# Kernel optimization log

Measured on AMD Instinct MI355X. Metric: run time of the kernel, lower is better.

Reference implementation:

```python
import jax, jax.numpy as jnp
import numpy as np
import math

PATCHES = [(2, 2), (4, 4), (8, 8), (16, 16)]  # (width, height) per scale
D_MODEL = 256
EPS = 1e-5


def setup_inputs() -> dict:
    key = jax.random.key(0)
    ks = jax.random.split(key, 12)
    b, c, h, w = 4, D_MODEL, 128, 128
    s = 1.0 / math.sqrt(c)
    inp = {
        'x': jax.random.normal(ks[0], (b, c, h, w), jnp.float32),
        'y': jax.random.normal(ks[1], (b, c, h, w), jnp.float32),
        'Wq': jax.random.normal(ks[2], (c, c), jnp.float32) * s,
        'bq': jnp.zeros((c,), jnp.float32),
        'Wk': jax.random.normal(ks[3], (c, c), jnp.float32) * s,
        'bk': jnp.zeros((c,), jnp.float32),
        'Wv': jax.random.normal(ks[4], (c, c), jnp.float32) * s,
        'bv': jnp.zeros((c,), jnp.float32),
        'Wo': jax.random.normal(ks[5], (c, c, 3, 3), jnp.float32) * (1.0 / math.sqrt(c * 9)),
        'bo': jnp.zeros((c,), jnp.float32),
        'gamma': jnp.ones((c,), jnp.float32),
        'beta': jnp.zeros((c,), jnp.float32),
    }
    return inp


def _conv1x1(x, W, b):
    # 1x1 conv == channel matmul
    return jnp.einsum('oc,bchw->bohw', W, x) + b[None, :, None, None]


def _windowed_attention(q, k, v, ww, hh):
    # q,k,v: [b, d_k, h, w] -> windows of (hh, ww), tokens = out_h*out_w
    b, d_k, h, w = q.shape
    out_h, out_w = h // hh, w // ww

    def to_tokens(t):
        t = t.reshape(b, d_k, out_h, hh, out_w, ww)
        t = t.transpose(0, 2, 4, 1, 3, 5)  # b, out_h, out_w, d_k, hh, ww
        return t.reshape(b, out_h * out_w, d_k * hh * ww)

    qt, kt, vt = to_tokens(q), to_tokens(k), to_tokens(v)
    scale = 1.0 / math.sqrt(qt.shape[-1])
    scores = jnp.einsum('bnd,bmd->bnm', qt, kt) * scale
    p = jax.nn.softmax(scores, axis=-1)
    out = jnp.einsum('bnm,bmd->bnd', p, vt)
    out = out.reshape(b, out_h, out_w, d_k, hh, ww)
    out = out.transpose(0, 3, 1, 4, 2, 5).reshape(b, d_k, h, w)
    return out


def reference(x, y, Wq, bq, Wk, bk, Wv, bv, Wo, bo, gamma, beta):
    b, c, h, w = x.shape
    n_scales = len(PATCHES)
    d_k = c // n_scales

    q_all = _conv1x1(x, Wq, bq)
    k_all = _conv1x1(y, Wk, bk)
    v_all = _conv1x1(y, Wv, bv)

    outs = []
    for i, (ww, hh) in enumerate(PATCHES):
        sl = slice(i * d_k, (i + 1) * d_k)
        outs.append(_windowed_attention(q_all[:, sl], k_all[:, sl], v_all[:, sl], ww, hh))
    out = jnp.concatenate(outs, axis=1)  # [b, c, h, w]

    # output_linear: Conv3x3 (pad 1) -> BatchNorm2d (batch stats) -> LeakyReLU(0.2)
    z = jax.lax.conv_general_dilated(
        out, Wo, window_strides=(1, 1), padding='SAME',
        dimension_numbers=('NCHW', 'OIHW', 'NCHW')) + bo[None, :, None, None]
    mean = jnp.mean(z, axis=(0, 2, 3), keepdims=True)
    var = jnp.var(z, axis=(0, 2, 3), keepdims=True)
    zn = (z - mean) * jax.lax.rsqrt(var + EPS)
    zn = zn * gamma[None, :, None, None] + beta[None, :, None, None]
    return jnp.where(zn >= 0, zn, 0.2 * zn)
```

## Files before the change

### kernel.cpp

```cpp
#include <hip/hip_runtime.h>
#include <math.h>

#define BN 4
#define CC 256
#define HH_ 128
#define WW_ 128
#define HWP (HH_*WW_)
#define TOK (64*HWP)


typedef __attribute__((ext_vector_type(8))) short bf16x8;
typedef __attribute__((ext_vector_type(4))) float f32x4;

__device__ __forceinline__ float bf2f(unsigned short u) {
    return __uint_as_float(((unsigned)u) << 16);
}
__device__ __forceinline__ unsigned short f2bf(float f) {
    unsigned u = __float_as_uint(f);
    u += 0x7FFF + ((u >> 16) & 1);
    return (unsigned short)(u >> 16);
}
__device__ __forceinline__ void load4f(const unsigned short* p, float o[4]) {
    ushort4 v = *(const ushort4*)p;
    o[0] = bf2f(v.x); o[1] = bf2f(v.y); o[2] = bf2f(v.z); o[3] = bf2f(v.w);
}
__device__ __forceinline__ float ld1(const unsigned short* p) { return bf2f(*p); }
__device__ __forceinline__ float ld1(const float* p) { return *p; }
__device__ __forceinline__ void st1(unsigned short* p, float v) { *p = f2bf(v); }
__device__ __forceinline__ void st1(float* p, float v) { *p = v; }

#define LDS_STRIDE 72

struct Tile32 { uint4 v[4]; };

__device__ __forceinline__ Tile32 load_tile_bf16(
    const unsigned short* src, size_t stride, int t)
{
    int r = t >> 1, kc = (t & 1) * 32;
    const uint4* sp = (const uint4*)(src + (size_t)r * stride + kc);
    Tile32 o;
    o.v[0] = sp[0]; o.v[1] = sp[1]; o.v[2] = sp[2]; o.v[3] = sp[3];
    return o;
}

__device__ __forceinline__ Tile32 load_tile_f32(
    const float* src, size_t stride, int t)
{
    int r = t >> 1, kc = (t & 1) * 32;
    const float4* sp = (const float4*)(src + (size_t)r * stride + kc);
    unsigned short tmp[32];
    #pragma unroll
    for (int i = 0; i < 8; i++) {
        float4 v = sp[i];
        tmp[i*4+0] = f2bf(v.x); tmp[i*4+1] = f2bf(v.y);
        tmp[i*4+2] = f2bf(v.z); tmp[i*4+3] = f2bf(v.w);
    }
    Tile32 o;
    const uint4* tp = (const uint4*)tmp;
    o.v[0] = tp[0]; o.v[1] = tp[1]; o.v[2] = tp[2]; o.v[3] = tp[3];
    return o;
}

__device__ __forceinline__ void store_tile(
    unsigned short* lds, const Tile32& d, int t)
{
    int r = t >> 1, kc = (t & 1) * 32;
    uint4* dp = (uint4*)&lds[r * LDS_STRIDE + kc];
    dp[0] = d.v[0]; dp[1] = d.v[1]; dp[2] = d.v[2]; dp[3] = d.v[3];
}

__device__ __forceinline__ void mfma_iter(
    const unsigned short* As, const unsigned short* Bs,
    int wm, int wn, int lr, int quad, f32x4 acc[4][4])
{
    #pragma unroll
    for (int s = 0; s < 2; s++) {
        bf16x8 af[4], bfr[4];
        #pragma unroll
        for (int i = 0; i < 4; i++)
            af[i] = *(const bf16x8*)&As[(wm*64 + i*16 + lr) * LDS_STRIDE + s*32 + quad*8];
        #pragma unroll
        for (int j = 0; j < 4; j++)
            bfr[j] = *(const bf16x8*)&Bs[(wn*64 + j*16 + lr) * LDS_STRIDE + s*32 + quad*8];
        #pragma unroll
        for (int i = 0; i < 4; i++)
            #pragma unroll
            for (int j = 0; j < 4; j++)
                acc[i][j] = __builtin_amdgcn_mfma_f32_16x16x32_bf16(
                    af[i], bfr[j], acc[i][j], 0, 0, 0);
    }
}

__global__ __launch_bounds__(256) void zero_kernel(float* __restrict__ p)
{
    p[blockIdx.x * 256 + threadIdx.x] = 0.f;
}

__global__ __launch_bounds__(256) void nchw_to_nhwc(
    const float* __restrict__ x, const float* __restrict__ y,
    unsigned short* __restrict__ xt, unsigned short* __restrict__ yt)
{
    __shared__ unsigned short T[64 * 72];
    int z = blockIdx.z;
    int b = z & 3, which = z >> 2;
    const float* src = (which ? y : x) + (size_t)b * CC * HWP;
    unsigned short* dst = (which ? yt : xt) + (size_t)b * HWP * CC;
    int p0 = blockIdx.x * 64, c0 = blockIdx.y * 64;
    int t = threadIdx.x;

    int cl = t >> 2, pc = (t & 3) * 16;
    #pragma unroll
    for (int e = 0; e < 16; e += 4) {
        float4 v = *(const float4*)&src[(size_t)(c0 + cl) * HWP + p0 + pc + e];
        T[(pc + e + 0) * 72 + cl] = f2bf(v.x);
        T[(pc + e + 1) * 72 + cl] = f2bf(v.y);
        T[(pc + e + 2) * 72 + cl] = f2bf(v.z);
        T[(pc + e + 3) * 72 + cl] = f2bf(v.w);
    }
    __syncthreads();
    int p = t >> 2, cc = (t & 3) * 16;
    uint4 a = *(uint4*)&T[p * 72 + cc];
    uint4 bsec = *(uint4*)&T[p * 72 + cc + 8];
    uint4* dp = (uint4*)&dst[(size_t)(p0 + p) * CC + c0 + cc];
    dp[0] = a; dp[1] = bsec;
}

__global__ __launch_bounds__(256) void wpack_kernel(
    const float* __restrict__ Wo, unsigned short* __restrict__ wpack)
{
    int o = blockIdx.x, c = threadIdx.x;
    const float* wr = Wo + ((size_t)o * CC + c) * 9;
    #pragma unroll
    for (int tap = 0; tap < 9; tap++)
        wpack[((size_t)o * 9 + tap) * CC + c] = f2bf(wr[tap]);
}

__global__ __launch_bounds__(256) void proj_gemm(
    const unsigned short* __restrict__ xt, const unsigned short* __restrict__ yt,
    const float* __restrict__ Wq, const float* __restrict__ bq,
    const float* __restrict__ Wk, const float* __restrict__ bk,
    const float* __restrict__ Wv, const float* __restrict__ bv,
    unsigned short* __restrict__ qt, unsigned short* __restrict__ kt,
    unsigned short* __restrict__ vt)
{
    __shared__ unsigned short As[128 * LDS_STRIDE], Bs[128 * LDS_STRIDE];
    int z = blockIdx.z, b = z & 3, which = z >> 2;
    const unsigned short* src = (which == 0) ? xt : yt;
    const float* Wm   = (which == 0) ? Wq : (which == 1 ? Wk : Wv);
    const float* bias = (which == 0) ? bq : (which == 1 ? bk : bv);
    unsigned short* outp = (which == 0) ? qt : (which == 1 ? kt : vt);

    int m0 = blockIdx.y * 128;
    int n0 = blockIdx.x * 128;
    const float* A = Wm + (size_t)m0 * CC;
    const unsigned short* B = src + ((size_t)b * HWP + n0) * CC;

    int t = threadIdx.x, w = t >> 6, lane = t & 63;
    int quad = lane >> 4, lr = lane & 15, wm = w >> 1, wn = w & 1;

    f32x4 acc[4][4];
    #pragma unroll
    for (int i = 0; i < 4; i++)
        #pragma unroll
        for (int j = 0; j < 4; j++) acc[i][j] = (f32x4){0.f, 0.f, 0.f, 0.f};

    for (int k0 = 0; k0 < CC; k0 += 64) {
        Tile32 ta = load_tile_f32(A + k0, CC, t);
        Tile32 tb = load_tile_bf16(B + k0, CC, t);
        __syncthreads();
        store_tile(As, ta, t); store_tile(Bs, tb, t);
        __syncthreads();
        mfma_iter(As, Bs, wm, wn, lr, quad, acc);
    }

    #pragma unroll
    for (int i = 0; i < 4; i++) {
        int obase = m0 + wm * 64 + i * 16 + quad * 4;
        #pragma unroll
        for (int rr = 0; rr < 4; rr++) {
            int o = obase + rr;
            int s = o >> 6, lg = s + 1;
            int ch = o & 63;
            float bia = bias[o];
            unsigned short* ob = outp + ((size_t)s * 4 + b) * TOK;
            #pragma unroll
            for (int j = 0; j < 4; j++) {
                int p = n0 + wn * 64 + j * 16 + lr;
                int yy = p >> 7, xx = p & 127;
                int oy = yy >> lg, wy = yy & ((1 << lg) - 1);
                int ox = xx >> lg, wx = xx & ((1 << lg) - 1);
                int tokn = (oy << (7 - lg)) + ox;
                int didx = (ch << (2 * lg)) + (wy << lg) + wx;
                size_t idx;
                if (which == 2 && s < 3)
                    idx = ((size_t)didx << (14 - 2 * lg)) + tokn;
                else
                    idx = ((size_t)tokn << (6 + 2 * lg)) + didx;
                ob[idx] = f2bf(acc[i][j][rr] + bia);
            }
        }
    }
}

#define PS_STRIDE 136

__global__ __launch_bounds__(512) void flash0(
    const unsigned short* __restrict__ qt, const unsigned short* __restrict__ kt,
    const unsigned short* __restrict__ vt, unsigned short* __restrict__ aot)
{
    __shared__ unsigned short Ps[64 * PS_STRIDE];
    __shared__ unsigned short Bs[256 * LDS_STRIDE];

    int L = blockIdx.x;
    int xcd = L & 7, slot = L >> 3;
    int b = xcd >> 1;
    int q0 = (slot + 32 * (xcd & 1)) * 64;

    const unsigned short* Qb = qt + (size_t)b * TOK;
    const unsigned short* Kb = kt + (size_t)b * TOK;
    const unsigned short* Vb = vt + (size_t)b * TOK;

    int t = threadIdx.x, w = t >> 6, lane = t & 63;
    int quad = lane >> 4, lr = lane & 15;
    int wm = w >> 2, wn = w & 3;

    bf16x8 aq[4][2][2];
    #pragma unroll
    for (int k = 0; k < 4; k++)
        #pragma unroll
        for (int s = 0; s < 2; s++)
            #pragma unroll
            for (int i = 0; i < 2; i++)
                aq[k][s][i] = *(const bf16x8*)&Qb[
                    (size_t)(q0 + wm*32 + i*16 + lr) * 256 + k*64 + s*32 + quad*8];

    f32x4 acc_o[2][4];
    #pragma unroll
    for (int i = 0; i < 2; i++)
        #pragma unroll
        for (int j = 0; j < 4; j++) acc_o[i][j] = (f32x4){0.f, 0.f, 0.f, 0.f};
    float rsum[2][4] = {};

    const float SC = 1.f / 16.f;
    int sr = t >> 1, sc_ = (t & 1) * 32;

    for (int kv0 = 0; kv0 < 4096; kv0 += 128) {
        f32x4 acc_s[2][2];
        #pragma unroll
        for (int i = 0; i < 2; i++)
            #pragma unroll
            for (int j = 0; j < 2; j++) acc_s[i][j] = (f32x4){0.f, 0.f, 0.f, 0.f};

        #pragma unroll
        for (int kp = 0; kp < 2; kp++) {
            __syncthreads();
            {
                const uint4* sp = (const uint4*)&Kb[
                    (size_t)(kv0 + (sr & 127)) * 256 + kp*128 + (sr >> 7)*64 + sc_];
                uint4* dp = (uint4*)&Bs[sr * LDS_STRIDE + sc_];
                dp[0] = sp[0]; dp[1] = sp[1]; dp[2] = sp[2]; dp[3] = sp[3];
            }
            __syncthreads();
            #pragma unroll
            for (int t2 = 0; t2 < 2; t2++)
                #pragma unroll
                for (int s = 0; s < 2; s++) {
                    bf16x8 bfr[2];
                    #pragma unroll
                    for (int j = 0; j < 2; j++)
                        bfr[j] = *(const bf16x8*)&Bs[
                            (t2*128 + wn*32 + j*16 + lr) * LDS_STRIDE + s*32 + quad*8];
                    #pragma unroll
                    for (int i = 0; i < 2; i++)
                        #pragma unroll
                        for (int j = 0; j < 2; j++)
                            acc_s[i][j] = __builtin_amdgcn_mfma_f32_16x16x32_bf16(
                                aq[kp*2 + t2][s][i], bfr[j], acc_s[i][j], 0, 0, 0);
                }
        }

        #pragma unroll
        for (int i = 0; i < 2; i++)
            #pragma unroll
            for (int j = 0; j < 2; j++)
                #pragma unroll
                for (int rr = 0; rr < 4; rr++) {
                    float e = __expf(acc_s[i][j][rr] * SC);
                    Ps[(wm*32 + i*16 + quad*4 + rr) * PS_STRIDE + wn*32 + j*16 + lr]
                        = f2bf(e);
                    rsum[i][rr] += e;
                }

        #pragma unroll
        for (int ks = 0; ks < 2; ks++) {
            __syncthreads();
            {
                const uint4* sp = (const uint4*)&Vb[
                    (size_t)sr * 4096 + kv0 + ks*64 + sc_];
                uint4* dp = (uint4*)&Bs[sr * LDS_STRIDE + sc_];
                dp[0] = sp[0]; dp[1] = sp[1]; dp[2] = sp[2]; dp[3] = sp[3];
            }
            __syncthreads();
            #pragma unroll
            for (int s = 0; s < 2; s++) {
                bf16x8 pa[2], vb[4];
                #pragma unroll
                for (int i = 0; i < 2; i++)
                    pa[i] = *(const bf16x8*)&Ps[
                        (wm*32 + i*16 + lr) * PS_STRIDE + ks*64 + s*32 + quad*8];
                #pragma unroll
                for (int j = 0; j < 4; j++)
                    vb[j] = *(const bf16x8*)&Bs[
                        (wn*64 + j*16 + lr) * LDS_STRIDE + s*32 + quad*8];
                #pragma unroll
                for (int i = 0; i < 2; i++)
                    #pragma unroll
                    for (int j = 0; j < 4; j++)
                        acc_o[i][j] = __builtin_amdgcn_mfma_f32_16x16x32_bf16(
                            pa[i], vb[j], acc_o[i][j], 0, 0, 0);
            }
        }
    }

    __syncthreads();
    float* rsred = (float*)Ps;
    #pragma unroll
    for (int i = 0; i < 2; i++)
        #pragma unroll
        for (int rr = 0; rr < 4; rr++) {
            float v = rsum[i][rr];
            v += __shfl_xor(v, 1); v += __shfl_xor(v, 2);
            v += __shfl_xor(v, 4); v += __shfl_xor(v, 8);
            if (lr == 0)
                rsred[wn*64 + wm*32 + i*16 + quad*4 + rr] = v;
        }
    __syncthreads();
    #pragma unroll
    for (int i = 0; i < 2; i++)
        #pragma unroll
        for (int rr = 0; rr < 4; rr++) {
            int tl = wm*32 + i*16 + quad*4 + rr;
            float inv = 1.f / (rsred[tl] + rsred[64 + tl]
                             + rsred[128 + tl] + rsred[192 + tl]);
            int tokn = q0 + tl;
            int oy = tokn >> 6, ox = tokn & 63;
            #pragma unroll
            for (int j = 0; j < 4; j++) {
                int d = wn*64 + j*16 + lr;
                int ch = d >> 2, wp = d & 3;
                int yy = oy*2 + (wp >> 1), xx = ox*2 + (wp & 1);
                aot[((size_t)b * HWP + yy * WW_ + xx) * CC + ch]
                    = f2bf(acc_o[i][j][rr] * inv);
            }
        }
}

template<int NTOK, int DD>
__global__ __launch_bounds__(256) void s_gemm_exp(
    const unsigned short* __restrict__ Qb, const unsigned short* __restrict__ Kb,
    unsigned short* __restrict__ S0, float* __restrict__ rsg, float sc)
{
    __shared__ unsigned short As[128 * LDS_STRIDE], Bs[128 * LDS_STRIDE];
    int bz = blockIdx.z;
    int m0 = blockIdx.y * 128, n0 = blockIdx.x * 128;
    const unsigned short* Q = Qb + (size_t)bz * TOK + (size_t)m0 * DD;
    const unsigned short* K = Kb + (size_t)bz * TOK + (size_t)n0 * DD;
    unsigned short* S = S0 + (size_t)bz * NTOK * NTOK;
    float* rs = rsg + (size_t)bz * NTOK;

    int t = threadIdx.x, w = t >> 6, lane = t & 63;
    int quad = lane >> 4, lr = lane & 15, wm = w >> 1, wn = w & 1;

    f32x4 acc[4][4];
    #pragma unroll
    for (int i = 0; i < 4; i++)
        #pragma unroll
        for (int j = 0; j < 4; j++) acc[i][j] = (f32x4){0.f, 0.f, 0.f, 0.f};

    for (int k0 = 0; k0 < DD; k0 += 64) {
        Tile32 ta = load_tile_bf16(Q + k0, DD, t);
        Tile32 tb = load_tile_bf16(K + k0, DD, t);
        __syncthreads();
        store_tile(As, ta, t); store_tile(Bs, tb, t);
        __syncthreads();
        mfma_iter(As, Bs, wm, wn, lr, quad, acc);
    }

    #pragma unroll
    for (int i = 0; i < 4; i++) {
        int m = m0 + wm * 64 + i * 16 + quad * 4;
        float rsum[4] = {0.f, 0.f, 0.f, 0.f};
        #pragma unroll
        for (int j = 0; j < 4; j++) {
            int n = n0 + wn * 64 + j * 16 + lr;
            #pragma unroll
            for (int rr = 0; rr < 4; rr++) {
                float e = __expf(acc[i][j][rr] * sc);
                S[(size_t)(m + rr) * NTOK + n] = f2bf(e);
                rsum[rr] += e;
            }
        }
        #pragma unroll
        for (int rr = 0; rr < 4; rr++) {
            float v = rsum[rr];
            v += __shfl_xor(v, 1);
            v += __shfl_xor(v, 2);
            v += __shfl_xor(v, 4);
            v += __shfl_xor(v, 8);
            if (lr == 0) atomicAdd(&rs[m + rr], v);
        }
    }
}

template<int NTOK, int DD, int LG, int CH0>
__global__ __launch_bounds__(256) void o_gemm(
    const unsigned short* __restrict__ Pb, const unsigned short* __restrict__ Vb,
    const float* __restrict__ rsg, unsigned short* __restrict__ aot, int b0)
{
    __shared__ unsigned short As[128 * LDS_STRIDE], Bs[128 * LDS_STRIDE];
    int bz = blockIdx.z, b = b0 + bz;
    int m0 = blockIdx.y * 128, n0 = blockIdx.x * 128;
    const unsigned short* P = Pb + (size_t)bz * NTOK * NTOK + (size_t)m0 * NTOK;
    const unsigned short* V = Vb + (size_t)bz * TOK + (size_t)n0 * NTOK;
    const float* rs = rsg + (size_t)bz * NTOK;

    int t = threadIdx.x, w = t >> 6, lane = t & 63;
    int quad = lane >> 4, lr = lane & 15, wm = w >> 1, wn = w & 1;

    f32x4 acc[4][4];
    #pragma unroll
    for (int i = 0; i < 4; i++)
        #pragma unroll
        for (int j = 0; j < 4; j++) acc[i][j] = (f32x4){0.f, 0.f, 0.f, 0.f};

    for (int k0 = 0; k0 < NTOK; k0 += 64) {
        Tile32 ta = load_tile_bf16(P + k0, NTOK, t);
        Tile32 tb = load_tile_bf16(V + k0, NTOK, t);
        __syncthreads();
        store_tile(As, ta, t); store_tile(Bs, tb, t);
        __syncthreads();
        mfma_iter(As, Bs, wm, wn, lr, quad, acc);
    }

    #pragma unroll
    for (int i = 0; i < 4; i++) {
        int tb0 = m0 + wm * 64 + i * 16 + quad * 4;
        #pragma unroll
        for (int rr = 0; rr < 4; rr++) {
            int tokn = tb0 + rr;
            float inv = 1.f / rs[tokn];
            int oy = tokn >> (7 - LG), ox = tokn & ((1 << (7 - LG)) - 1);
            #pragma unroll
            for (int j = 0; j < 4; j++) {
                int d = n0 + wn * 64 + j * 16 + lr;
                int ch = d >> (2 * LG);
                int r2 = d & ((1 << (2 * LG)) - 1);
                int wy = r2 >> LG, wx = r2 & ((1 << LG) - 1);
                int yy = (oy << LG) + wy, xx = (ox << LG) + wx;
                aot[((size_t)b * HWP + yy * WW_ + xx) * CC + CH0 + ch] =
                    f2bf(acc[i][j][rr] * inv);
            }
        }
    }
}

__global__ __launch_bounds__(256) void s2_partial(
    const unsigned short* __restrict__ Qb, const unsigned short* __restrict__ Kb,
    float* __restrict__ S2p)
{
    __shared__ unsigned short As[128 * LDS_STRIDE], Bs[128 * LDS_STRIDE];
    int z = blockIdx.z, b = z >> 3, sp = z & 7;
    int m0 = blockIdx.y * 128, n0 = blockIdx.x * 128;
    const unsigned short* Q = Qb + (size_t)b * TOK + (size_t)m0 * 4096;
    const unsigned short* K = Kb + (size_t)b * TOK + (size_t)n0 * 4096;
    float* So = S2p + ((size_t)(sp * 4 + b)) * 65536;

    int t = threadIdx.x, w = t >> 6, lane = t & 63;
    int quad = lane >> 4, lr = lane & 15, wm = w >> 1, wn = w & 1;

    f32x4 acc[4][4];
    #pragma unroll
    for (int i = 0; i < 4; i++)
        #pragma unroll
        for (int j = 0; j < 4; j++) acc[i][j] = (f32x4){0.f, 0.f, 0.f, 0.f};

    int kend = sp * 512 + 512;
    for (int k0 = sp * 512; k0 < kend; k0 += 64) {
        Tile32 ta = load_tile_bf16(Q + k0, 4096, t);
        Tile32 tb = load_tile_bf16(K + k0, 4096, t);
        __syncthreads();
        store_tile(As, ta, t); store_tile(Bs, tb, t);
        __syncthreads();
        mfma_iter(As, Bs, wm, wn, lr, quad, acc);
    }

    #pragma unroll
    for (int i = 0; i < 4; i++) {
        int m = m0 + wm * 64 + i * 16 + quad * 4;
        #pragma unroll
        for (int j = 0; j < 4; j++) {
            int n = n0 + wn * 64 + j * 16 + lr;
            #pragma unroll
            for (int rr = 0; rr < 4; rr++)
                So[(size_t)(m + rr) * 256 + n] = acc[i][j][rr];
        }
    }
}

__global__ __launch_bounds__(256) void s2_finish(
    const float* __restrict__ S2p, unsigned short* __restrict__ Sbf,
    float* __restrict__ rs2, float sc)
{
    int row = blockIdx.x, b = blockIdx.y, t = threadIdx.x;
    float v = 0.f;
    #pragma unroll
    for (int sp = 0; sp < 8; sp++)
        v += S2p[((size_t)(sp * 4 + b)) * 65536 + row * 256 + t];
    float e = __expf(v * sc);
    Sbf[((size_t)b * 65536) + row * 256 + t] = f2bf(e);
    __shared__ float red[256];
    red[t] = e; __syncthreads();
    for (int s = 128; s > 0; s >>= 1) {
        if (t < s) red[t] += red[t + s];
        __syncthreads();
    }
    if (t == 0) rs2[b * 256 + row] = red[0];
}

__device__ __forceinline__ Tile32 load_tile_conv(
    const unsigned short* aob, int ys, int dx, int cbase, int t)
{
    int r = t >> 1, kc = (t & 1) * 32;
    int xs = r + dx;
    Tile32 o;
    if (ys >= 0 && ys < HH_ && xs >= 0 && xs < WW_) {
        const uint4* sp = (const uint4*)(aob + ((size_t)ys * WW_ + xs) * CC + cbase + kc);
        o.v[0] = sp[0]; o.v[1] = sp[1]; o.v[2] = sp[2]; o.v[3] = sp[3];
    } else {
        uint4 zz = make_uint4(0, 0, 0, 0);
        o.v[0] = zz; o.v[1] = zz; o.v[2] = zz; o.v[3] = zz;
    }
    return o;
}

__global__ __launch_bounds__(256) void conv_gemm(
    const unsigned short* __restrict__ aot, const unsigned short* __restrict__ wpack,
    const float* __restrict__ bo, float* __restrict__ zout,
    float* __restrict__ stats)
{
    __shared__ unsigned short As[128 * LDS_STRIDE], Bs[128 * LDS_STRIDE];
    int yrow = blockIdx.x;
    int o0 = blockIdx.y * 128;
    int b = blockIdx.z;
    const unsigned short* aob = aot + (size_t)b * HWP * CC;
    const unsigned short* wsrc = wpack + (size_t)o0 * 2304;

    int t = threadIdx.x, w = t >> 6, lane = t & 63;
    int quad = lane >> 4, lr = lane & 15, wm = w >> 1, wn = w & 1;

    f32x4 acc[4][4];
    #pragma unroll
    for (int i = 0; i < 4; i++)
        #pragma unroll
        for (int j = 0; j < 4; j++) acc[i][j] = (f32x4){0.f, 0.f, 0.f, 0.f};

    for (int tap = 0; tap < 9; tap++) {
        int dy = tap / 3 - 1, dx = tap % 3 - 1;
        int ys = yrow + dy;
        for (int cb = 0; cb < CC; cb += 64) {
            Tile32 ta = load_tile_bf16(wsrc + tap * CC + cb, 2304, t);
            Tile32 tb = load_tile_conv(aob, ys, dx, cb, t);
            __syncthreads();
            store_tile(As, ta, t); store_tile(Bs, tb, t);
            __syncthreads();
            mfma_iter(As, Bs, wm, wn, lr, quad, acc);
        }
    }

    #pragma unroll
    for (int i = 0; i < 4; i++) {
        #pragma unroll
        for (int rr = 0; rr < 4; rr++) {
            int o = o0 + wm * 64 + i * 16 + quad * 4 + rr;
            float bia = bo[o];
            float s1 = 0.f, s2v = 0.f;
            #pragma unroll
            for (int j = 0; j < 4; j++) {
                int x = wn * 64 + j * 16 + lr;
                float v = acc[i][j][rr] + bia;
                zout[((size_t)(b * CC + o)) * HWP + yrow * WW_ + x] = v;
                s1 += v; s2v = fmaf(v, v, s2v);
            }
            s1 += __shfl_xor(s1, 1); s2v += __shfl_xor(s2v, 1);
            s1 += __shfl_xor(s1, 2); s2v += __shfl_xor(s2v, 2);
            s1 += __shfl_xor(s1, 4); s2v += __shfl_xor(s2v, 4);
            s1 += __shfl_xor(s1, 8); s2v += __shfl_xor(s2v, 8);
            if (lr == 0) {
                atomicAdd(&stats[o], s1);
                atomicAdd(&stats[CC + o], s2v);
            }
        }
    }
}

__global__ __launch_bounds__(256) void stats_finalize(
    float* __restrict__ stats, const float* __restrict__ gamma,
    const float* __restrict__ beta)
{
    int c = threadIdx.x;
    const float inv_n = 1.f / (BN * HWP);
    float mean = stats[c] * inv_n;
    float var = stats[CC + c] * inv_n - mean * mean;
    float rstd = rsqrtf(var + 1e-5f);
    float gs = gamma[c] * rstd;
    stats[c] = gs;
    stats[CC + c] = beta[c] - mean * gs;
}

__global__ __launch_bounds__(256) void s3_kernel(
    const unsigned short* __restrict__ Qb, const unsigned short* __restrict__ Kb,
    float* __restrict__ S, float sc)
{
    const int N = 64, D = 16384, KLEN = 1024;
    int b = blockIdx.z >> 4, kc = blockIdx.z & 15;
    const unsigned short* Q = Qb + (size_t)b * TOK;
    const unsigned short* K = Kb + (size_t)b * TOK;
    float* Sb = S + (size_t)b * N * N;
    int k0 = kc * KLEN;

    __shared__ float As[16][64], Bs[16][64];
    int t = threadIdx.x, tx = t & 15, ty = t >> 4, r = t >> 2, q = t & 3;

    float acc[4][4] = {};
    for (int kk = k0; kk < k0 + KLEN; kk += 16) {
        float a4[4], b4[4];
        load4f(&Q[(size_t)r * D + kk + q * 4], a4);
        load4f(&K[(size_t)r * D + kk + q * 4], b4);
        __syncthreads();
        As[q*4+0][r] = a4[0]; As[q*4+1][r] = a4[1]; As[q*4+2][r] = a4[2]; As[q*4+3][r] = a4[3];
        Bs[q*4+0][r] = b4[0]; Bs[q*4+1][r] = b4[1]; Bs[q*4+2][r] = b4[2]; Bs[q*4+3][r] = b4[3];
        __syncthreads();
        #pragma unroll
        for (int k = 0; k < 16; k++) {
            float4 af = *(const float4*)&As[k][ty*4];
            float4 bf = *(const float4*)&Bs[k][tx*4];
            float ar[4] = {af.x, af.y, af.z, af.w};
            float br[4] = {bf.x, bf.y, bf.z, bf.w};
            #pragma unroll
            for (int ii = 0; ii < 4; ii++)
                #pragma unroll
                for (int jj = 0; jj < 4; jj++)
                    acc[ii][jj] = fmaf(ar[ii], br[jj], acc[ii][jj]);
        }
    }

    #pragma unroll
    for (int ii = 0; ii < 4; ii++)
        #pragma unroll
        for (int jj = 0; jj < 4; jj++)
            atomicAdd(&Sb[(size_t)(ty * 4 + ii) * N + tx * 4 + jj], acc[ii][jj] * sc);
}

template<typename T>
__global__ __launch_bounds__(256) void softmax_kernel(T* __restrict__ S, int n)
{
    int b = blockIdx.y;
    int row = blockIdx.x;
    T* rp = S + (size_t)b * n * n + (size_t)row * n;
    __shared__ float red[256];
    int t = threadIdx.x;

    float m = -1e30f;
    for (int j = t; j < n; j += 256) m = fmaxf(m, ld1(&rp[j]));
    red[t] = m; __syncthreads();
    for (int s = 128; s > 0; s >>= 1) { if (t < s) red[t] = fmaxf(red[t], red[t + s]); __syncthreads(); }
    m = red[0]; __syncthreads();

    float sum = 0.f;
    for (int j = t; j < n; j += 256) { float e = __expf(ld1(&rp[j]) - m); st1(&rp[j], e); sum += e; }
    red[t] = sum; __syncthreads();
    for (int s = 128; s > 0; s >>= 1) { if (t < s) red[t] += red[t + s]; __syncthreads(); }
    float inv = 1.f / red[0];
    for (int j = t; j < n; j += 256) st1(&rp[j], ld1(&rp[j]) * inv);
}

__global__ __launch_bounds__(256) void o3_kernel(
    const float* __restrict__ P, const unsigned short* __restrict__ Vb,
    unsigned short* __restrict__ aot)
{
    const int N = 64, D = 16384, LG = 4, CH0 = 192;
    int bz = blockIdx.z;
    const float* Pb = P + (size_t)bz * N * N;
    const unsigned short* V = Vb + (size_t)bz * TOK;
    int i0 = blockIdx.x * 64, d0 = blockIdx.y * 64;

    __shared__ float Ps[16][64];
    __shared__ float Vs[16][64];
    int t = threadIdx.x, tx = t & 15, ty = t >> 4, r = t >> 2, q = t & 3;
    int vr = t >> 4, vq = t & 15;

    float acc[4][4] = {};
    for (int j0 = 0; j0 < N; j0 += 16) {
        float p4[4], v4[4];
        float4 pv = *(const float4*)&Pb[(size_t)(i0 + r) * N + j0 + q * 4];
        p4[0] = pv.x; p4[1] = pv.y; p4[2] = pv.z; p4[3] = pv.w;
        load4f(&V[(size_t)(j0 + vr) * D + d0 + vq * 4], v4);
        __syncthreads();
        Ps[q*4+0][r] = p4[0]; Ps[q*4+1][r] = p4[1]; Ps[q*4+2][r] = p4[2]; Ps[q*4+3][r] = p4[3];
        Vs[vr][vq*4+0] = v4[0]; Vs[vr][vq*4+1] = v4[1]; Vs[vr][vq*4+2] = v4[2]; Vs[vr][vq*4+3] = v4[3];
        __syncthreads();
        #pragma unroll
        for (int k = 0; k < 16; k++) {
            float4 pf = *(const float4*)&Ps[k][ty*4];
            float4 vf = *(const float4*)&Vs[k][tx*4];
            float pr[4] = {pf.x, pf.y, pf.z, pf.w};
            float vrr[4] = {vf.x, vf.y, vf.z, vf.w};
            #pragma unroll
            for (int ii = 0; ii < 4; ii++)
                #pragma unroll
                for (int jj = 0; jj < 4; jj++)
                    acc[ii][jj] = fmaf(pr[ii], vrr[jj], acc[ii][jj]);
        }
    }

    #pragma unroll
    for (int ii = 0; ii < 4; ii++) {
        int tokn = i0 + ty * 4 + ii;
        int oy = tokn >> (7 - LG), ox = tokn & ((1 << (7 - LG)) - 1);
        #pragma unroll
        for (int jj = 0; jj < 4; jj++) {
            int d = d0 + tx * 4 + jj;
            int ch = d >> (2 * LG);
            int r2 = d & ((1 << (2 * LG)) - 1);
            int wy = r2 >> LG, wx = r2 & ((1 << LG) - 1);
            int yy = (oy << LG) + wy, xx = (ox << LG) + wx;
            aot[((size_t)bz * HWP + yy * WW_ + xx) * CC + CH0 + ch] = f2bf(acc[ii][jj]);
        }
    }
}

__global__ __launch_bounds__(256) void bn_apply_kernel(
    float* __restrict__ z, const float* __restrict__ stats)
{
    size_t i4 = (size_t)blockIdx.x * 256 + threadIdx.x;
    size_t idx = i4 * 4;
    int c = (int)((idx >> 14) & 255);
    float gs = stats[c], gb = stats[CC + c];
    float4 v = *(float4*)&z[idx];
    v.x = fmaf(v.x, gs, gb); v.y = fmaf(v.y, gs, gb);
    v.z = fmaf(v.z, gs, gb); v.w = fmaf(v.w, gs, gb);
    v.x = v.x >= 0.f ? v.x : 0.2f * v.x;
    v.y = v.y >= 0.f ? v.y : 0.2f * v.y;
    v.z = v.z >= 0.f ? v.z : 0.2f * v.z;
    v.w = v.w >= 0.f ? v.w : 0.2f * v.w;
    *(float4*)&z[idx] = v;
}

extern "C" void kernel_launch(void* const* d_in, const int* in_sizes, int n_in,
                              void* d_out, int out_size, void* d_ws, size_t ws_size,
                              hipStream_t stream)
{
    const float* x     = (const float*)d_in[0];
    const float* y     = (const float*)d_in[1];
    const float* Wq    = (const float*)d_in[2];
    const float* bq    = (const float*)d_in[3];
    const float* Wk    = (const float*)d_in[4];
    const float* bk    = (const float*)d_in[5];
    const float* Wv    = (const float*)d_in[6];
    const float* bv    = (const float*)d_in[7];
    const float* Wo    = (const float*)d_in[8];
    const float* bo    = (const float*)d_in[9];
    const float* gamma = (const float*)d_in[10];
    const float* beta  = (const float*)d_in[11];
    float* out = (float*)d_out;

    unsigned short* qt    = (unsigned short*)d_ws;
    unsigned short* kt    = qt + (size_t)16777216;
    unsigned short* vt    = kt + (size_t)16777216;
    unsigned short* aot   = vt + (size_t)16777216;
    unsigned short* Sbf   = aot + (size_t)16777216;
    unsigned short* wpack = Sbf + (size_t)16777216;
    float* stats = (float*)(wpack + (size_t)589824);
    float* S3    = stats + 512;
    float* rs0   = S3 + 16384;
    float* rs1   = rs0 + 16384;
    float* rs2   = rs1 + 4096;
    (void)rs0;
    unsigned short* xt = Sbf;
    unsigned short* yt = aot;
    float* S2p = (float*)d_out;

    dim3 blk(256);

    zero_kernel<<<dim3(150), blk, 0, stream>>>(stats);
    nchw_to_nhwc<<<dim3(256, 4, 8), blk, 0, stream>>>(x, y, xt, yt);
    wpack_kernel<<<dim3(256), blk, 0, stream>>>(Wo, wpack);

    proj_gemm<<<dim3(128, 2, 12), blk, 0, stream>>>(
        xt, yt, Wq, bq, Wk, bk, Wv, bv, qt, kt, vt);

    flash0<<<dim3(256), dim3(512), 0, stream>>>(qt, kt, vt, aot);

    s_gemm_exp<1024, 1024><<<dim3(8, 8, 4), blk, 0, stream>>>(
        qt + (size_t)4 * TOK, kt + (size_t)4 * TOK, Sbf, rs1, 1.f / 32.f);
    o_gemm<1024, 1024, 2, 64><<<dim3(8, 8, 4), blk, 0, stream>>>(
        Sbf, vt + (size_t)4 * TOK, rs1, aot, 0);

    s2_partial<<<dim3(2, 2, 32), blk, 0, stream>>>(
        qt + (size_t)8 * TOK, kt + (size_t)8 * TOK, S2p);
    s2_finish<<<dim3(256, 4), blk, 0, stream>>>(S2p, Sbf, rs2, 1.f / 64.f);
    o_gemm<256, 4096, 3, 128><<<dim3(32, 2, 4), blk, 0, stream>>>(
        Sbf, vt + (size_t)8 * TOK, rs2, aot, 0);

    s3_kernel<<<dim3(1, 1, 64), blk, 0, stream>>>(
        qt + (size_t)12 * TOK, kt + (size_t)12 * TOK, S3, 1.f / 128.f);
    softmax_kernel<float><<<dim3(64, 4), blk, 0, stream>>>(S3, 64);
    o3_kernel<<<dim3(1, 256, 4), blk, 0, stream>>>(S3, vt + (size_t)12 * TOK, aot);

    conv_gemm<<<dim3(128, 2, 4), blk, 0, stream>>>(aot, wpack, bo, out, stats);
    stats_finalize<<<dim3(1), blk, 0, stream>>>(stats, gamma, beta);
    bn_apply_kernel<<<dim3(16384), blk, 0, stream>>>(out, stats);
}
```

Before: 880.2 us.

## Use async LDS loads with swizzle, double-buffer GEMMs, split flash0 over KV

The GEMM kernels now load tiles with global_load_lds straight into XOR-swizzled, double-buffered LDS, so the next tile's fetch overlaps the current MFMA work. The QKV weights are pre-converted to bf16 by a new pack kernel so the projection can use the same path. flash0 is split into two KV halves across twice as many blocks, writing fp32 partials and atomically summed row sums, with a new combine kernel that normalises and scatters the output. This aims to cut load latency, bank conflicts and occupancy limits, but adds fp32 partial traffic, atomics and an extra launch.

```diff
diff --git a/kernel.cpp b/kernel.cpp
--- a/kernel.cpp
+++ b/kernel.cpp
@@ -29,6 +29,53 @@
 __device__ __forceinline__ void st1(unsigned short* p, float v) { *p = f2bf(v); }
 __device__ __forceinline__ void st1(float* p, float v) { *p = v; }
 
+__device__ __forceinline__ void gload16(const void* g, void* l) {
+    __builtin_amdgcn_global_load_lds(
+        (__attribute__((address_space(1))) void*)(g),
+        (__attribute__((address_space(3))) void*)(l), 16, 0, 0);
+}
+
+__device__ __forceinline__ void stage64(
+    const unsigned short* src, size_t strideElems, unsigned short* lds, int t)
+{
+    #pragma unroll
+    for (int k = 0; k < 4; k++) {
+        int n = t + k * 256;
+        int row = n >> 3, slot = n & 7;
+        const char* gp = (const char*)(src + (size_t)row * strideElems)
+                       + ((slot ^ (row & 7)) << 4);
+        gload16(gp, (char*)lds + n * 16);
+    }
+}
+
+__device__ __forceinline__ void mfma_iter_swz(
+    const unsigned short* As, const unsigned short* Bs,
+    int wm, int wn, int lr, int quad, f32x4 acc[4][4])
+{
+    #pragma unroll
+    for (int s = 0; s < 2; s++) {
+        bf16x8 af[4], bfr[4];
+        #pragma unroll
+        for (int i = 0; i < 4; i++) {
+            int row = wm*64 + i*16 + lr;
+            int off = (row << 7) + (s << 6) + (quad << 4);
+            af[i] = *(const bf16x8*)((const char*)As + (off ^ ((row & 7) << 4)));
+        }
+        #pragma unroll
+        for (int j = 0; j < 4; j++) {
+            int row = wn*64 + j*16 + lr;
+            int off = (row << 7) + (s << 6) + (quad << 4);
+            bfr[j] = *(const bf16x8*)((const char*)Bs + (off ^ ((row & 7) << 4)));
+        }
+        #pragma unroll
+        for (int i = 0; i < 4; i++)
+            #pragma unroll
+            for (int j = 0; j < 4; j++)
+                acc[i][j] = __builtin_amdgcn_mfma_f32_16x16x32_bf16(
+                    af[i], bfr[j], acc[i][j], 0, 0, 0);
+    }
+}
+
 #define LDS_STRIDE 72
 
 struct Tile32 { uint4 v[4]; };
@@ -40,24 +87,6 @@
     const uint4* sp = (const uint4*)(src + (size_t)r * stride + kc);
     Tile32 o;
     o.v[0] = sp[0]; o.v[1] = sp[1]; o.v[2] = sp[2]; o.v[3] = sp[3];
-    return o;
-}
-
-__device__ __forceinline__ Tile32 load_tile_f32(
-    const float* src, size_t stride, int t)
-{
-    int r = t >> 1, kc = (t & 1) * 32;
-    const float4* sp = (const float4*)(src + (size_t)r * stride + kc);
-    unsigned short tmp[32];
-    #pragma unroll
-    for (int i = 0; i < 8; i++) {
-        float4 v = sp[i];
-        tmp[i*4+0] = f2bf(v.x); tmp[i*4+1] = f2bf(v.y);
-        tmp[i*4+2] = f2bf(v.z); tmp[i*4+3] = f2bf(v.w);
-    }
-    Tile32 o;
-    const uint4* tp = (const uint4*)tmp;
-    o.v[0] = tp[0]; o.v[1] = tp[1]; o.v[2] = tp[2]; o.v[3] = tp[3];
     return o;
 }
 
@@ -135,24 +164,34 @@
         wpack[((size_t)o * 9 + tap) * CC + c] = f2bf(wr[tap]);
 }
 
+__global__ __launch_bounds__(256) void wqkv_pack(
+    const float* __restrict__ Wq, const float* __restrict__ Wk,
+    const float* __restrict__ Wv, unsigned short* __restrict__ Wb)
+{
+    int which = blockIdx.x;
+    const float* W = which == 0 ? Wq : (which == 1 ? Wk : Wv);
+    unsigned short* o = Wb + (size_t)which * 65536;
+    for (int i = threadIdx.x; i < 65536; i += 256)
+        o[i] = f2bf(W[i]);
+}
+
 __global__ __launch_bounds__(256) void proj_gemm(
     const unsigned short* __restrict__ xt, const unsigned short* __restrict__ yt,
-    const float* __restrict__ Wq, const float* __restrict__ bq,
-    const float* __restrict__ Wk, const float* __restrict__ bk,
-    const float* __restrict__ Wv, const float* __restrict__ bv,
+    const unsigned short* __restrict__ Wqkv,
+    const float* __restrict__ bq, const float* __restrict__ bk,
+    const float* __restrict__ bv,
     unsigned short* __restrict__ qt, unsigned short* __restrict__ kt,
     unsigned short* __restrict__ vt)
 {
-    __shared__ unsigned short As[128 * LDS_STRIDE], Bs[128 * LDS_STRIDE];
+    __shared__ unsigned short Asb[2][8192], Bsb[2][8192];
     int z = blockIdx.z, b = z & 3, which = z >> 2;
     const unsigned short* src = (which == 0) ? xt : yt;
-    const float* Wm   = (which == 0) ? Wq : (which == 1 ? Wk : Wv);
     const float* bias = (which == 0) ? bq : (which == 1 ? bk : bv);
     unsigned short* outp = (which == 0) ? qt : (which == 1 ? kt : vt);
 
     int m0 = blockIdx.y * 128;
     int n0 = blockIdx.x * 128;
-    const float* A = Wm + (size_t)m0 * CC;
+    const unsigned short* A = Wqkv + (size_t)which * 65536 + (size_t)m0 * CC;
     const unsigned short* B = src + ((size_t)b * HWP + n0) * CC;
 
     int t = threadIdx.x, w = t >> 6, lane = t & 63;
@@ -164,13 +203,18 @@
         #pragma unroll
         for (int j = 0; j < 4; j++) acc[i][j] = (f32x4){0.f, 0.f, 0.f, 0.f};
 
+    stage64(A, CC, Asb[0], t);
+    stage64(B, CC, Bsb[0], t);
+    __syncthreads();
+    int cur = 0;
     for (int k0 = 0; k0 < CC; k0 += 64) {
-        Tile32 ta = load_tile_f32(A + k0, CC, t);
-        Tile32 tb = load_tile_bf16(B + k0, CC, t);
+        if (k0 + 64 < CC) {
+            stage64(A + k0 + 64, CC, Asb[cur ^ 1], t);
+            stage64(B + k0 + 64, CC, Bsb[cur ^ 1], t);
+        }
+        mfma_iter_swz(Asb[cur], Bsb[cur], wm, wn, lr, quad, acc);
         __syncthreads();
-        store_tile(As, ta, t); store_tile(Bs, tb, t);
-        __syncthreads();
-        mfma_iter(As, Bs, wm, wn, lr, quad, acc);
+        cur ^= 1;
     }
 
     #pragma unroll
@@ -206,15 +250,19 @@
 
 __global__ __launch_bounds__(512) void flash0(
     const unsigned short* __restrict__ qt, const unsigned short* __restrict__ kt,
-    const unsigned short* __restrict__ vt, unsigned short* __restrict__ aot)
+    const unsigned short* __restrict__ vt, float* __restrict__ part,
+    float* __restrict__ rs0g)
 {
     __shared__ unsigned short Ps[64 * PS_STRIDE];
-    __shared__ unsigned short Bs[256 * LDS_STRIDE];
+    __shared__ unsigned short Bs[256 * 64];
 
     int L = blockIdx.x;
     int xcd = L & 7, slot = L >> 3;
     int b = xcd >> 1;
-    int q0 = (slot + 32 * (xcd & 1)) * 64;
+    int idx = slot + 64 * (xcd & 1);
+    int h = idx >> 6;
+    int q0 = (idx & 63) * 64;
+    int kvbase = h * 2048;
 
     const unsigned short* Qb = qt + (size_t)b * TOK;
     const unsigned short* Kb = kt + (size_t)b * TOK;
@@ -242,9 +290,8 @@
     float rsum[2][4] = {};
 
     const float SC = 1.f / 16.f;
-    int sr = t >> 1, sc_ = (t & 1) * 32;
-
-    for (int kv0 = 0; kv0 < 4096; kv0 += 128) {
+
+    for (int kv0 = kvbase; kv0 < kvbase + 2048; kv0 += 128) {
         f32x4 acc_s[2][2];
         #pragma unroll
         for (int i = 0; i < 2; i++)
@@ -254,22 +301,29 @@
         #pragma unroll
         for (int kp = 0; kp < 2; kp++) {
             __syncthreads();
-            {
-                const uint4* sp = (const uint4*)&Kb[
-                    (size_t)(kv0 + (sr & 127)) * 256 + kp*128 + (sr >> 7)*64 + sc_];
-                uint4* dp = (uint4*)&Bs[sr * LDS_STRIDE + sc_];
-                dp[0] = sp[0]; dp[1] = sp[1]; dp[2] = sp[2]; dp[3] = sp[3];
+            #pragma unroll
+            for (int k = 0; k < 4; k++) {
+                int n = t + k * 512;
+                int R = n >> 3, sl = n & 7;
+                int kl = R & 127, dsub = R >> 7;
+                const char* gp = (const char*)(Kb + (size_t)(kv0 + kl) * 256
+                                 + kp*128 + dsub*64) + ((sl ^ (R & 7)) << 4);
+                gload16(gp, (char*)Bs + n * 16);
             }
             __syncthreads();
+            __builtin_amdgcn_s_setprio(1);
             #pragma unroll
             for (int t2 = 0; t2 < 2; t2++)
                 #pragma unroll
                 for (int s = 0; s < 2; s++) {
                     bf16x8 bfr[2];
                     #pragma unroll
-                    for (int j = 0; j < 2; j++)
-                        bfr[j] = *(const bf16x8*)&Bs[
-                            (t2*128 + wn*32 + j*16 + lr) * LDS_STRIDE + s*32 + quad*8];
+                    for (int j = 0; j < 2; j++) {
+                        int row = t2*128 + wn*32 + j*16 + lr;
+                        int off = (row << 7) + (s << 6) + (quad << 4);
+                        bfr[j] = *(const bf16x8*)((const char*)Bs
+                                   + (off ^ ((row & 7) << 4)));
+                    }
                     #pragma unroll
                     for (int i = 0; i < 2; i++)
                         #pragma unroll
@@ -277,6 +331,7 @@
                             acc_s[i][j] = __builtin_amdgcn_mfma_f32_16x16x32_bf16(
                                 aq[kp*2 + t2][s][i], bfr[j], acc_s[i][j], 0, 0, 0);
                 }
+            __builtin_amdgcn_s_setprio(0);
         }
 
         #pragma unroll
@@ -294,13 +349,16 @@
         #pragma unroll
         for (int ks = 0; ks < 2; ks++) {
             __syncthreads();
-            {
-                const uint4* sp = (const uint4*)&Vb[
-                    (size_t)sr * 4096 + kv0 + ks*64 + sc_];
-                uint4* dp = (uint4*)&Bs[sr * LDS_STRIDE + sc_];
-                dp[0] = sp[0]; dp[1] = sp[1]; dp[2] = sp[2]; dp[3] = sp[3];
+            #pragma unroll
+            for (int k = 0; k < 4; k++) {
+                int n = t + k * 512;
+                int R = n >> 3, sl = n & 7;
+                const char* gp = (const char*)(Vb + (size_t)R * 4096 + kv0 + ks*64)
+                               + ((sl ^ (R & 7)) << 4);
+                gload16(gp, (char*)Bs + n * 16);
             }
             __syncthreads();
+            __builtin_amdgcn_s_setprio(1);
             #pragma unroll
             for (int s = 0; s < 2; s++) {
                 bf16x8 pa[2], vb[4];
@@ -309,9 +367,12 @@
                     pa[i] = *(const bf16x8*)&Ps[
                         (wm*32 + i*16 + lr) * PS_STRIDE + ks*64 + s*32 + quad*8];
                 #pragma unroll
-                for (int j = 0; j < 4; j++)
-                    vb[j] = *(const bf16x8*)&Bs[
-                        (wn*64 + j*16 + lr) * LDS_STRIDE + s*32 + quad*8];
+                for (int j = 0; j < 4; j++) {
+                    int row = wn*64 + j*16 + lr;
+                    int off = (row << 7) + (s << 6) + (quad << 4);
+                    vb[j] = *(const bf16x8*)((const char*)Bs
+                              + (off ^ ((row & 7) << 4)));
+                }
                 #pragma unroll
                 for (int i = 0; i < 2; i++)
                     #pragma unroll
@@ -319,11 +380,10 @@
                         acc_o[i][j] = __builtin_amdgcn_mfma_f32_16x16x32_bf16(
                             pa[i], vb[j], acc_o[i][j], 0, 0, 0);
             }
-        }
-    }
-
-    __syncthreads();
-    float* rsred = (float*)Ps;
+            __builtin_amdgcn_s_setprio(0);
+        }
+    }
+
     #pragma unroll
     for (int i = 0; i < 2; i++)
         #pragma unroll
@@ -332,27 +392,41 @@
             v += __shfl_xor(v, 1); v += __shfl_xor(v, 2);
             v += __shfl_xor(v, 4); v += __shfl_xor(v, 8);
             if (lr == 0)
-                rsred[wn*64 + wm*32 + i*16 + quad*4 + rr] = v;
-        }
-    __syncthreads();
+                atomicAdd(&rs0g[b * 4096 + q0 + wm*32 + i*16 + quad*4 + rr], v);
+        }
+    float* op = part + ((size_t)(h * 4 + b)) * TOK;
     #pragma unroll
     for (int i = 0; i < 2; i++)
         #pragma unroll
         for (int rr = 0; rr < 4; rr++) {
-            int tl = wm*32 + i*16 + quad*4 + rr;
-            float inv = 1.f / (rsred[tl] + rsred[64 + tl]
-                             + rsred[128 + tl] + rsred[192 + tl]);
-            int tokn = q0 + tl;
-            int oy = tokn >> 6, ox = tokn & 63;
-            #pragma unroll
-            for (int j = 0; j < 4; j++) {
-                int d = wn*64 + j*16 + lr;
-                int ch = d >> 2, wp = d & 3;
-                int yy = oy*2 + (wp >> 1), xx = ox*2 + (wp & 1);
-                aot[((size_t)b * HWP + yy * WW_ + xx) * CC + ch]
-                    = f2bf(acc_o[i][j][rr] * inv);
-            }
-        }
+            int tokl = wm*32 + i*16 + quad*4 + rr;
+            float* orow = op + (size_t)(q0 + tokl) * 256;
+            #pragma unroll
+            for (int j = 0; j < 4; j++)
+                orow[wn*64 + j*16 + lr] = acc_o[i][j][rr];
+        }
+}
+
+__global__ __launch_bounds__(256) void combine0f(
+    const float* __restrict__ part, const float* __restrict__ rs,
+    unsigned short* __restrict__ aot)
+{
+    int b = blockIdx.y;
+    int tok0 = blockIdx.x * 16;
+    const float* p0 = part + (size_t)b * TOK;
+    const float* p1 = part + (size_t)(4 + b) * TOK;
+    int t = threadIdx.x;
+    int w = t >> 6, ch = t & 63;
+    int wy = w >> 1, wx = w & 1;
+    #pragma unroll 4
+    for (int u = 0; u < 16; u++) {
+        int tok = tok0 + u;
+        size_t base = (size_t)tok * 256 + ch * 4 + w;
+        float v = (p0[base] + p1[base]) * (1.f / rs[b * 4096 + tok]);
+        int oy = tok >> 6, ox = tok & 63;
+        int yy = oy * 2 + wy, xx = ox * 2 + wx;
+        aot[((size_t)b * HWP + yy * WW_ + xx) * CC + ch] = f2bf(v);
+    }
 }
 
 template<int NTOK, int DD>
@@ -360,7 +434,7 @@
     const unsigned short* __restrict__ Qb, const unsigned short* __restrict__ Kb,
     unsigned short* __restrict__ S0, float* __restrict__ rsg, float sc)
 {
-    __shared__ unsigned short As[128 * LDS_STRIDE], Bs[128 * LDS_STRIDE];
+    __shared__ unsigned short Asb[2][8192], Bsb[2][8192];
     int bz = blockIdx.z;
     int m0 = blockIdx.y * 128, n0 = blockIdx.x * 128;
     const unsigned short* Q = Qb + (size_t)bz * TOK + (size_t)m0 * DD;
@@ -377,13 +451,18 @@
         #pragma unroll
         for (int j = 0; j < 4; j++) acc[i][j] = (f32x4){0.f, 0.f, 0.f, 0.f};
 
+    stage64(Q, DD, Asb[0], t);
+    stage64(K, DD, Bsb[0], t);
+    __syncthreads();
+    int cur = 0;
     for (int k0 = 0; k0 < DD; k0 += 64) {
-        Tile32 ta = load_tile_bf16(Q + k0, DD, t);
-        Tile32 tb = load_tile_bf16(K + k0, DD, t);
+        if (k0 + 64 < DD) {
+            stage64(Q + k0 + 64, DD, Asb[cur ^ 1], t);
+            stage64(K + k0 + 64, DD, Bsb[cur ^ 1], t);
+        }
+        mfma_iter_swz(Asb[cur], Bsb[cur], wm, wn, lr, quad, acc);
         __syncthreads();
-        store_tile(As, ta, t); store_tile(Bs, tb, t);
-        __syncthreads();
-        mfma_iter(As, Bs, wm, wn, lr, quad, acc);
+        cur ^= 1;
     }
 
     #pragma unroll
@@ -417,7 +496,7 @@
     const unsigned short* __restrict__ Pb, const unsigned short* __restrict__ Vb,
     const float* __restrict__ rsg, unsigned short* __restrict__ aot, int b0)
 {
-    __shared__ unsigned short As[128 * LDS_STRIDE], Bs[128 * LDS_STRIDE];
+    __shared__ unsigned short Asb[2][8192], Bsb[2][8192];
     int bz = blockIdx.z, b = b0 + bz;
     int m0 = blockIdx.y * 128, n0 = blockIdx.x * 128;
     const unsigned short* P = Pb + (size_t)bz * NTOK * NTOK + (size_t)m0 * NTOK;
@@ -433,13 +512,18 @@
         #pragma unroll
         for (int j = 0; j < 4; j++) acc[i][j] = (f32x4){0.f, 0.f, 0.f, 0.f};
 
+    stage64(P, NTOK, Asb[0], t);
+    stage64(V, NTOK, Bsb[0], t);
+    __syncthreads();
+    int cur = 0;
     for (int k0 = 0; k0 < NTOK; k0 += 64) {
-        Tile32 ta = load_tile_bf16(P + k0, NTOK, t);
-        Tile32 tb = load_tile_bf16(V + k0, NTOK, t);
+        if (k0 + 64 < NTOK) {
+            stage64(P + k0 + 64, NTOK, Asb[cur ^ 1], t);
+            stage64(V + k0 + 64, NTOK, Bsb[cur ^ 1], t);
+        }
+        mfma_iter_swz(Asb[cur], Bsb[cur], wm, wn, lr, quad, acc);
         __syncthreads();
-        store_tile(As, ta, t); store_tile(Bs, tb, t);
-        __syncthreads();
-        mfma_iter(As, Bs, wm, wn, lr, quad, acc);
+        cur ^= 1;
     }
 
     #pragma unroll
@@ -468,11 +552,11 @@
     const unsigned short* __restrict__ Qb, const unsigned short* __restrict__ Kb,
     float* __restrict__ S2p)
 {
-    __shared__ unsigned short As[128 * LDS_STRIDE], Bs[128 * LDS_STRIDE];
+    __shared__ unsigned short Asb[2][8192], Bsb[2][8192];
     int z = blockIdx.z, b = z >> 3, sp = z & 7;
     int m0 = blockIdx.y * 128, n0 = blockIdx.x * 128;
-    const unsigned short* Q = Qb + (size_t)b * TOK + (size_t)m0 * 4096;
-    const unsigned short* K = Kb + (size_t)b * TOK + (size_t)n0 * 4096;
+    const unsigned short* Q = Qb + (size_t)b * TOK + (size_t)m0 * 4096 + sp * 512;
+    const unsigned short* K = Kb + (size_t)b * TOK + (size_t)n0 * 4096 + sp * 512;
     float* So = S2p + ((size_t)(sp * 4 + b)) * 65536;
 
     int t = threadIdx.x, w = t >> 6, lane = t & 63;
@@ -484,14 +568,18 @@
         #pragma unroll
         for (int j = 0; j < 4; j++) acc[i][j] = (f32x4){0.f, 0.f, 0.f, 0.f};
 
-    int kend = sp * 512 + 512;
-    for (int k0 = sp * 512; k0 < kend; k0 += 64) {
-        Tile32 ta = load_tile_bf16(Q + k0, 4096, t);
-        Tile32 tb = load_tile_bf16(K + k0, 4096, t);
+    stage64(Q, 4096, Asb[0], t);
+    stage64(K, 4096, Bsb[0], t);
+    __syncthreads();
+    int cur = 0;
+    for (int k0 = 0; k0 < 512; k0 += 64) {
+        if (k0 + 64 < 512) {
+            stage64(Q + k0 + 64, 4096, Asb[cur ^ 1], t);
+            stage64(K + k0 + 64, 4096, Bsb[cur ^ 1], t);
+        }
+        mfma_iter_swz(Asb[cur], Bsb[cur], wm, wn, lr, quad, acc);
         __syncthreads();
-        store_tile(As, ta, t); store_tile(Bs, tb, t);
-        __syncthreads();
-        mfma_iter(As, Bs, wm, wn, lr, quad, acc);
+        cur ^= 1;
     }
 
     #pragma unroll
@@ -785,9 +873,10 @@
     float* rs0   = S3 + 16384;
     float* rs1   = rs0 + 16384;
     float* rs2   = rs1 + 4096;
-    (void)rs0;
     unsigned short* xt = Sbf;
     unsigned short* yt = aot;
+    float* part = (float*)d_out;
+    unsigned short* Wqkv_bf = (unsigned short*)((char*)d_out + (size_t)33554432);
     float* S2p = (float*)d_out;
 
     dim3 blk(256);
@@ -795,11 +884,13 @@
     zero_kernel<<<dim3(150), blk, 0, stream>>>(stats);
     nchw_to_nhwc<<<dim3(256, 4, 8), blk, 0, stream>>>(x, y, xt, yt);
     wpack_kernel<<<dim3(256), blk, 0, stream>>>(Wo, wpack);
+    wqkv_pack<<<dim3(3), blk, 0, stream>>>(Wq, Wk, Wv, Wqkv_bf);
 
     proj_gemm<<<dim3(128, 2, 12), blk, 0, stream>>>(
-        xt, yt, Wq, bq, Wk, bk, Wv, bv, qt, kt, vt);
-
-    flash0<<<dim3(256), dim3(512), 0, stream>>>(qt, kt, vt, aot);
+        xt, yt, Wqkv_bf, bq, bk, bv, qt, kt, vt);
+
+    flash0<<<dim3(512), dim3(512), 0, stream>>>(qt, kt, vt, part, rs0);
+    combine0f<<<dim3(256, 4), blk, 0, stream>>>(part, rs0, aot);
 
     s_gemm_exp<1024, 1024><<<dim3(8, 8, 4), blk, 0, stream>>>(
         qt + (size_t)4 * TOK, kt + (size_t)4 * TOK, Sbf, rs1, 1.f / 32.f);
```

New measurement: 870.5 us. No clear change (-1.1%).
